# Kernel optimization log

Hardware: AMD Instinct MI355X
Metric: run time of the kernel (lower is better)

Reference implementation:

```python
import jax, jax.numpy as jnp
import numpy as np

FORCE = 8.0
N_STATE = 40
BATCH = 524288


def setup_inputs() -> dict:
    key = jax.random.key(0)
    x0 = jax.random.normal(key, (BATCH, N_STATE), dtype=jnp.float32)
    t = jnp.float32(0.0)          # unused: system is autonomous (torch code passes nan)
    dt = jnp.float32(0.05)        # canonical Lorenz96 RK4 step
    return {"x0": x0, "t": t, "dt": dt}


def _dxdt(x):
    # torch shift(x, n) == roll(x, -n, dims=-1)
    # dxdt = (shift(x,1) - shift(x,-2)) * shift(x,-1) - x + force
    return (jnp.roll(x, -1, axis=-1) - jnp.roll(x, 2, axis=-1)) * jnp.roll(x, 1, axis=-1) - x + FORCE


def reference(x0, t, dt):
    # Classic RK4 step (rk4_torch); t is ignored (autonomous RHS).
    k1 = _dxdt(x0)
    k2 = _dxdt(x0 + 0.5 * dt * k1)
    k3 = _dxdt(x0 + 0.5 * dt * k2)
    k4 = _dxdt(x0 + dt * k3)
    return x0 + (dt / 6.0) * (k1 + 2.0 * k2 + 2.0 * k3 + k4)
```

## Files before the change

kernel.cpp:

```cpp
#include <hip/hip_runtime.h>


#define FORCE 8.0f

__global__ __launch_bounds__(256)
void lorenz96_rk4_shfl(const float4* __restrict__ x0,
                       const float* __restrict__ dt_p,
                       float4* __restrict__ out,
                       long nf4)
{
    const long tid  = (long)blockIdx.x * blockDim.x + threadIdx.x;
    const long wave = tid >> 6;
    const int  lane = (int)(tid & 63);
    const int  lrow = lane / 10;
    const int  c    = lane - lrow * 10;
    const long f    = wave * 60 + lane;
    const bool active = (lane < 60) && (f < nf4);

    const int lL = lrow * 10 + (c == 0 ? 9 : c - 1);
    const int lR = lrow * 10 + (c == 9 ? 0 : c + 1);

    const float dt  = dt_p[0];
    const float hdt = 0.5f * dt;

    float4 v = make_float4(0.f, 0.f, 0.f, 0.f);
    if (active) v = x0[f];
    const float x0r = v.x, x1r = v.y, x2r = v.z, x3r = v.w;

    auto deriv = [&](float s0, float s1, float s2, float s3,
                     float& d0, float& d1, float& d2, float& d3) {
        float hL2 = __shfl(s2, lL);
        float hL3 = __shfl(s3, lL);
        float hR0 = __shfl(s0, lR);
        d0 = (s1  - hL2) * hL3 - s0 + FORCE;
        d1 = (s2  - hL3) * s0  - s1 + FORCE;
        d2 = (s3  - s0 ) * s1  - s2 + FORCE;
        d3 = (hR0 - s1 ) * s2  - s3 + FORCE;
    };

    float k0, k1, k2, k3;
    float a0, a1, a2, a3;
    float y0, y1, y2, y3;

    deriv(x0r, x1r, x2r, x3r, k0, k1, k2, k3);
    a0 = k0; a1 = k1; a2 = k2; a3 = k3;
    y0 = x0r + hdt * k0; y1 = x1r + hdt * k1;
    y2 = x2r + hdt * k2; y3 = x3r + hdt * k3;

    deriv(y0, y1, y2, y3, k0, k1, k2, k3);
    a0 += 2.0f * k0; a1 += 2.0f * k1; a2 += 2.0f * k2; a3 += 2.0f * k3;
    y0 = x0r + hdt * k0; y1 = x1r + hdt * k1;
    y2 = x2r + hdt * k2; y3 = x3r + hdt * k3;

    deriv(y0, y1, y2, y3, k0, k1, k2, k3);
    a0 += 2.0f * k0; a1 += 2.0f * k1; a2 += 2.0f * k2; a3 += 2.0f * k3;
    y0 = x0r + dt * k0; y1 = x1r + dt * k1;
    y2 = x2r + dt * k2; y3 = x3r + dt * k3;

    deriv(y0, y1, y2, y3, k0, k1, k2, k3);
    a0 += k0; a1 += k1; a2 += k2; a3 += k3;

    const float s = dt * (1.0f / 6.0f);
    float4 r;
    r.x = x0r + s * a0;
    r.y = x1r + s * a1;
    r.z = x2r + s * a2;
    r.w = x3r + s * a3;
    if (active) out[f] = r;
}

extern "C" void kernel_launch(void* const* d_in, const int* in_sizes, int n_in,
                              void* d_out, int out_size, void* d_ws, size_t ws_size,
                              hipStream_t stream) {
    const float4* x0 = (const float4*)d_in[0];
    const float* dt = (const float*)d_in[2];
    float4* out = (float4*)d_out;

    const long nf4 = (long)in_sizes[0] / 4;
    const long nwaves = (nf4 + 59) / 60;
    const int block = 256;
    const long grid = (nwaves + 3) / 4;
    lorenz96_rk4_shfl<<<dim3((unsigned)grid), dim3(block), 0, stream>>>(x0, dt, out, nf4);
}
```

Measured before the change: 145.9 us.

## Give each thread half a row and exchange halo values via DPP lane swap

Each thread now owns 20 consecutive state elements (half of a 40-wide row) and loads them as five float4s. Paired lanes trade their boundary values with a DPP quad_perm swap instead of ds_bpermute shuffles, and no lanes sit idle in the 60-of-64 scheme. The intent is to cut cross-lane traffic and wasted lanes. The cost is higher register use per thread and strided per-thread loads: adjacent threads touch addresses 80 bytes apart, so coalescing is looser.

```diff
diff --git a/kernel.cpp b/kernel.cpp
--- a/kernel.cpp
+++ b/kernel.cpp
@@ -3,70 +3,70 @@
 
 #define FORCE 8.0f
 
+__device__ __forceinline__ float dpp_swap1(float x) {
+    return __int_as_float(
+        __builtin_amdgcn_mov_dpp(__float_as_int(x), 0xB1, 0xF, 0xF, true));
+}
+
 __global__ __launch_bounds__(256)
-void lorenz96_rk4_shfl(const float4* __restrict__ x0,
-                       const float* __restrict__ dt_p,
-                       float4* __restrict__ out,
-                       long nf4)
+void lorenz96_rk4_dpp(const float4* __restrict__ x0,
+                      const float* __restrict__ dt_p,
+                      float4* __restrict__ out,
+                      long nhalf)
 {
-    const long tid  = (long)blockIdx.x * blockDim.x + threadIdx.x;
-    const long wave = tid >> 6;
-    const int  lane = (int)(tid & 63);
-    const int  lrow = lane / 10;
-    const int  c    = lane - lrow * 10;
-    const long f    = wave * 60 + lane;
-    const bool active = (lane < 60) && (f < nf4);
-
-    const int lL = lrow * 10 + (c == 0 ? 9 : c - 1);
-    const int lR = lrow * 10 + (c == 9 ? 0 : c + 1);
+    const long tid = (long)blockIdx.x * blockDim.x + threadIdx.x;
+    if (tid >= nhalf) return;
+    const long base = tid * 5;
 
     const float dt  = dt_p[0];
     const float hdt = 0.5f * dt;
 
-    float4 v = make_float4(0.f, 0.f, 0.f, 0.f);
-    if (active) v = x0[f];
-    const float x0r = v.x, x1r = v.y, x2r = v.z, x3r = v.w;
+    float x[20];
+#pragma unroll
+    for (int j = 0; j < 5; ++j) {
+        float4 v = x0[base + j];
+        x[4*j+0] = v.x; x[4*j+1] = v.y; x[4*j+2] = v.z; x[4*j+3] = v.w;
+    }
 
-    auto deriv = [&](float s0, float s1, float s2, float s3,
-                     float& d0, float& d1, float& d2, float& d3) {
-        float hL2 = __shfl(s2, lL);
-        float hL3 = __shfl(s3, lL);
-        float hR0 = __shfl(s0, lR);
-        d0 = (s1  - hL2) * hL3 - s0 + FORCE;
-        d1 = (s2  - hL3) * s0  - s1 + FORCE;
-        d2 = (s3  - s0 ) * s1  - s2 + FORCE;
-        d3 = (hR0 - s1 ) * s2  - s3 + FORCE;
-    };
+    float s[20], k[20], a[20];
 
-    float k0, k1, k2, k3;
-    float a0, a1, a2, a3;
-    float y0, y1, y2, y3;
+#define DERIV(S, D)                                                          \
+    {                                                                        \
+        const float hm2 = dpp_swap1(S[18]);                                  \
+        const float hm1 = dpp_swap1(S[19]);                                  \
+        const float hp1 = dpp_swap1(S[0]);                                   \
+        D[0] = (S[1] - hm2) * hm1 - S[0] + FORCE;                            \
+        D[1] = (S[2] - hm1) * S[0] - S[1] + FORCE;                           \
+        _Pragma("unroll")                                                    \
+        for (int i = 2; i < 19; ++i)                                         \
+            D[i] = (S[i+1] - S[i-2]) * S[i-1] - S[i] + FORCE;                \
+        D[19] = (hp1 - S[17]) * S[18] - S[19] + FORCE;                       \
+    }
 
-    deriv(x0r, x1r, x2r, x3r, k0, k1, k2, k3);
-    a0 = k0; a1 = k1; a2 = k2; a3 = k3;
-    y0 = x0r + hdt * k0; y1 = x1r + hdt * k1;
-    y2 = x2r + hdt * k2; y3 = x3r + hdt * k3;
+    DERIV(x, k);
+#pragma unroll
+    for (int i = 0; i < 20; ++i) { a[i] = k[i];        s[i] = fmaf(hdt, k[i], x[i]); }
+    DERIV(s, k);
+#pragma unroll
+    for (int i = 0; i < 20; ++i) { a[i] += 2.0f*k[i];  s[i] = fmaf(hdt, k[i], x[i]); }
+    DERIV(s, k);
+#pragma unroll
+    for (int i = 0; i < 20; ++i) { a[i] += 2.0f*k[i];  s[i] = fmaf(dt,  k[i], x[i]); }
+    DERIV(s, k);
+#pragma unroll
+    for (int i = 0; i < 20; ++i) { a[i] += k[i]; }
 
-    deriv(y0, y1, y2, y3, k0, k1, k2, k3);
-    a0 += 2.0f * k0; a1 += 2.0f * k1; a2 += 2.0f * k2; a3 += 2.0f * k3;
-    y0 = x0r + hdt * k0; y1 = x1r + hdt * k1;
-    y2 = x2r + hdt * k2; y3 = x3r + hdt * k3;
-
-    deriv(y0, y1, y2, y3, k0, k1, k2, k3);
-    a0 += 2.0f * k0; a1 += 2.0f * k1; a2 += 2.0f * k2; a3 += 2.0f * k3;
-    y0 = x0r + dt * k0; y1 = x1r + dt * k1;
-    y2 = x2r + dt * k2; y3 = x3r + dt * k3;
-
-    deriv(y0, y1, y2, y3, k0, k1, k2, k3);
-    a0 += k0; a1 += k1; a2 += k2; a3 += k3;
-
-    const float s = dt * (1.0f / 6.0f);
-    float4 r;
-    r.x = x0r + s * a0;
-    r.y = x1r + s * a1;
-    r.z = x2r + s * a2;
-    r.w = x3r + s * a3;
-    if (active) out[f] = r;
+    const float sc = dt * (1.0f / 6.0f);
+#pragma unroll
+    for (int j = 0; j < 5; ++j) {
+        float4 r;
+        r.x = fmaf(sc, a[4*j+0], x[4*j+0]);
+        r.y = fmaf(sc, a[4*j+1], x[4*j+1]);
+        r.z = fmaf(sc, a[4*j+2], x[4*j+2]);
+        r.w = fmaf(sc, a[4*j+3], x[4*j+3]);
+        out[base + j] = r;
+    }
+#undef DERIV
 }
 
 extern "C" void kernel_launch(void* const* d_in, const int* in_sizes, int n_in,
@@ -76,9 +76,8 @@
     const float* dt = (const float*)d_in[2];
     float4* out = (float4*)d_out;
 
-    const long nf4 = (long)in_sizes[0] / 4;
-    const long nwaves = (nf4 + 59) / 60;
+    const long nhalf = (long)in_sizes[0] / 20;
     const int block = 256;
-    const long grid = (nwaves + 3) / 4;
-    lorenz96_rk4_shfl<<<dim3((unsigned)grid), dim3(block), 0, stream>>>(x0, dt, out, nf4);
+    const long grid = (nhalf + block - 1) / block;
+    lorenz96_rk4_dpp<<<dim3((unsigned)grid), dim3(block), 0, stream>>>(x0, dt, out, nhalf);
 }
```

Measured after the change: 156.8 us. +7.5%, slower.

## Replace lane shuffles with redundant halo loads and recompute of RK4 stages

Applied to the files above, without the earlier changes.

Each thread now loads its own float4 plus three neighbouring float4s of the same row (halo) and recomputes the RK4 stages on a shrinking stencil window, removing all cross-lane shuffles and the dependencies between lanes at each stage. It trades the shuffle latency for four times the global loads (mostly cache hits) and extra redundant arithmetic plus higher register use. The kernel is memory-bound, so the extra loads could add pressure on L1/L2.

```diff
diff --git a/kernel.cpp b/kernel.cpp
--- a/kernel.cpp
+++ b/kernel.cpp
@@ -4,7 +4,7 @@
 #define FORCE 8.0f
 
 __global__ __launch_bounds__(256)
-void lorenz96_rk4_shfl(const float4* __restrict__ x0,
+void lorenz96_rk4_halo(const float4* __restrict__ x0,
                        const float* __restrict__ dt_p,
                        float4* __restrict__ out,
                        long nf4)
@@ -15,58 +15,72 @@
     const int  lrow = lane / 10;
     const int  c    = lane - lrow * 10;
     const long f    = wave * 60 + lane;
-    const bool active = (lane < 60) && (f < nf4);
+    if (lane >= 60 || f >= nf4) return;
 
-    const int lL = lrow * 10 + (c == 0 ? 9 : c - 1);
-    const int lR = lrow * 10 + (c == 9 ? 0 : c + 1);
+    const long rowbase = wave * 60 + (long)lrow * 10;
+    const int cm2 = (c >= 2) ? c - 2 : c + 8;
+    const int cm1 = (c >= 1) ? c - 1 : c + 9;
+    const int cp1 = (c <= 8) ? c + 1 : c - 9;
+
+    const float4 vm2 = x0[rowbase + cm2];
+    const float4 vm1 = x0[rowbase + cm1];
+    const float4 v0  = x0[rowbase + c  ];
+    const float4 vp1 = x0[rowbase + cp1];
+
+    float xa[16];
+    xa[0]=vm2.x; xa[1]=vm2.y; xa[2]=vm2.z; xa[3]=vm2.w;
+    xa[4]=vm1.x; xa[5]=vm1.y; xa[6]=vm1.z; xa[7]=vm1.w;
+    xa[8]=v0.x;  xa[9]=v0.y;  xa[10]=v0.z; xa[11]=v0.w;
+    xa[12]=vp1.x; xa[13]=vp1.y; xa[14]=vp1.z; xa[15]=vp1.w;
 
     const float dt  = dt_p[0];
     const float hdt = 0.5f * dt;
 
-    float4 v = make_float4(0.f, 0.f, 0.f, 0.f);
-    if (active) v = x0[f];
-    const float x0r = v.x, x1r = v.y, x2r = v.z, x3r = v.w;
 
-    auto deriv = [&](float s0, float s1, float s2, float s3,
-                     float& d0, float& d1, float& d2, float& d3) {
-        float hL2 = __shfl(s2, lL);
-        float hL3 = __shfl(s3, lL);
-        float hR0 = __shfl(s0, lR);
-        d0 = (s1  - hL2) * hL3 - s0 + FORCE;
-        d1 = (s2  - hL3) * s0  - s1 + FORCE;
-        d2 = (s3  - s0 ) * s1  - s2 + FORCE;
-        d3 = (hR0 - s1 ) * s2  - s3 + FORCE;
-    };
+    float k1[13], y1[13];
+#pragma unroll
+    for (int i = 0; i < 13; ++i)
+        k1[i] = (xa[i+3] - xa[i]) * xa[i+1] - xa[i+2] + FORCE;
+#pragma unroll
+    for (int i = 0; i < 13; ++i)
+        y1[i] = fmaf(hdt, k1[i], xa[i+2]);
 
-    float k0, k1, k2, k3;
-    float a0, a1, a2, a3;
-    float y0, y1, y2, y3;
+    float k2[10], y2[10];
+#pragma unroll
+    for (int i = 0; i < 10; ++i)
+        k2[i] = (y1[i+3] - y1[i]) * y1[i+1] - y1[i+2] + FORCE;
+#pragma unroll
+    for (int i = 0; i < 10; ++i)
+        y2[i] = fmaf(hdt, k2[i], xa[i+4]);
 
-    deriv(x0r, x1r, x2r, x3r, k0, k1, k2, k3);
-    a0 = k0; a1 = k1; a2 = k2; a3 = k3;
-    y0 = x0r + hdt * k0; y1 = x1r + hdt * k1;
-    y2 = x2r + hdt * k2; y3 = x3r + hdt * k3;
+    float k3[7], y3[7];
+#pragma unroll
+    for (int i = 0; i < 7; ++i)
+        k3[i] = (y2[i+3] - y2[i]) * y2[i+1] - y2[i+2] + FORCE;
+#pragma unroll
+    for (int i = 0; i < 7; ++i)
+        y3[i] = fmaf(dt, k3[i], xa[i+6]);
 
-    deriv(y0, y1, y2, y3, k0, k1, k2, k3);
-    a0 += 2.0f * k0; a1 += 2.0f * k1; a2 += 2.0f * k2; a3 += 2.0f * k3;
-    y0 = x0r + hdt * k0; y1 = x1r + hdt * k1;
-    y2 = x2r + hdt * k2; y3 = x3r + hdt * k3;
+    float k4[4];
+#pragma unroll
+    for (int i = 0; i < 4; ++i)
+        k4[i] = (y3[i+3] - y3[i]) * y3[i+1] - y3[i+2] + FORCE;
 
-    deriv(y0, y1, y2, y3, k0, k1, k2, k3);
-    a0 += 2.0f * k0; a1 += 2.0f * k1; a2 += 2.0f * k2; a3 += 2.0f * k3;
-    y0 = x0r + dt * k0; y1 = x1r + dt * k1;
-    y2 = x2r + dt * k2; y3 = x3r + dt * k3;
-
-    deriv(y0, y1, y2, y3, k0, k1, k2, k3);
-    a0 += k0; a1 += k1; a2 += k2; a3 += k3;
-
-    const float s = dt * (1.0f / 6.0f);
+    const float sc = dt * (1.0f / 6.0f);
+    float acc[4];
+#pragma unroll
+    for (int m = 0; m < 4; ++m) {
+        float t = k1[m+6] + k4[m];
+        t = fmaf(2.0f, k2[m+4], t);
+        t = fmaf(2.0f, k3[m+2], t);
+        acc[m] = t;
+    }
     float4 r;
-    r.x = x0r + s * a0;
-    r.y = x1r + s * a1;
-    r.z = x2r + s * a2;
-    r.w = x3r + s * a3;
-    if (active) out[f] = r;
+    r.x = fmaf(sc, acc[0], xa[8]);
+    r.y = fmaf(sc, acc[1], xa[9]);
+    r.z = fmaf(sc, acc[2], xa[10]);
+    r.w = fmaf(sc, acc[3], xa[11]);
+    out[f] = r;
 }
 
 extern "C" void kernel_launch(void* const* d_in, const int* in_sizes, int n_in,
@@ -80,5 +94,5 @@
     const long nwaves = (nf4 + 59) / 60;
     const int block = 256;
     const long grid = (nwaves + 3) / 4;
-    lorenz96_rk4_shfl<<<dim3((unsigned)grid), dim3(block), 0, stream>>>(x0, dt, out, nf4);
+    lorenz96_rk4_halo<<<dim3((unsigned)grid), dim3(block), 0, stream>>>(x0, dt, out, nf4);
 }
```

Measured after the change: 149.1 us. 2.2% more time.
